# Performance work log

Hardware: AMD Instinct MI355X
Metric: run time of the kernel (lower is better)

## Reference

```python
import jax, jax.numpy as jnp
import numpy as np

EMB = 1024
HEADS = 16
DH = EMB // HEADS


def setup_inputs() -> dict:
    key = jax.random.key(0)
    ks = jax.random.split(key, 9)
    B, S = 4, 2048
    scale = 1.0 / np.sqrt(EMB)
    x = jax.random.normal(ks[0], (B, S, EMB), dtype=jnp.float32)
    Wq = jax.random.normal(ks[1], (EMB, EMB), dtype=jnp.float32) * scale
    Wk = jax.random.normal(ks[2], (EMB, EMB), dtype=jnp.float32) * scale
    Wv = jax.random.normal(ks[3], (EMB, EMB), dtype=jnp.float32) * scale
    Wo = jax.random.normal(ks[4], (EMB, EMB), dtype=jnp.float32) * scale
    bq = jnp.zeros((EMB,), jnp.float32)
    bk = jnp.zeros((EMB,), jnp.float32)
    bv = jnp.zeros((EMB,), jnp.float32)
    bo = jnp.zeros((EMB,), jnp.float32)
    return {"x": x, "Wq": Wq, "bq": bq, "Wk": Wk, "bk": bk,
            "Wv": Wv, "bv": bv, "Wo": Wo, "bo": bo}


def _split_heads(t):
    B, S, _ = t.shape
    return t.reshape(B, S, HEADS, DH).transpose(0, 2, 1, 3)  # [B,H,S,Dh]


def reference(x, Wq, bq, Wk, bk, Wv, bv, Wo, bo):
    q = _split_heads(x @ Wq + bq)
    k = _split_heads(x @ Wk + bk)
    v = _split_heads(x @ Wv + bv)
    # scaled dot-product attention, full [B,H,S,S] score matrix as in source
    logits = jnp.einsum("bhqd,bhkd->bhqk", q, k) / jnp.sqrt(jnp.float32(DH))
    attn = jax.nn.softmax(logits, axis=-1)
    ctx = jnp.einsum("bhqk,bhkd->bhqd", attn, v)
    B, _, S, _ = ctx.shape
    concat = ctx.transpose(0, 2, 1, 3).reshape(B, S, EMB)
    return concat @ Wo + bo
```

## Files before the change

### kernel.cpp

```cpp
#include <hip/hip_runtime.h>
#include <hip/hip_bf16.h>
#include <stdint.h>

typedef __bf16 bf16;
typedef __bf16 bf16x4 __attribute__((ext_vector_type(4)));
typedef __bf16 bf16x8 __attribute__((ext_vector_type(8)));
typedef float f32x4 __attribute__((ext_vector_type(4)));

__device__ __forceinline__ void async_ld16(const void* g, void* l) {
  __builtin_amdgcn_global_load_lds(
      (__attribute__((address_space(1))) void*)(void*)(g),
      (__attribute__((address_space(3))) void*)(l), 16, 0, 0);
}

__device__ __forceinline__ bf16 fast_bf16(float f) {
  uint32_t u = (__float_as_uint(f) + 0x8000u) >> 16;
  union { uint16_t s; bf16 b; } cv;
  cv.s = (uint16_t)u;
  return cv.b;
}

__device__ __forceinline__ uint32_t pack_bf16(float lo, float hi) {
  return __builtin_amdgcn_perm(__float_as_uint(hi) + 0x8000u,
                               __float_as_uint(lo) + 0x8000u, 0x07060302u);
}

__global__ __launch_bounds__(256) void cast_f32_bf16(const float* __restrict__ in,
                                                     bf16* __restrict__ out, int n) {
  int i = (blockIdx.x * 256 + threadIdx.x) * 4;
  if (i < n) {
    float4 f = *(const float4*)(in + i);
    uint2 o;
    o.x = pack_bf16(f.x, f.y);
    o.y = pack_bf16(f.z, f.w);
    *(uint2*)(out + i) = o;
  }
}

__global__ __launch_bounds__(256) void transpose_weights(const float* __restrict__ Wq,
                                                         const float* __restrict__ Wk,
                                                         const float* __restrict__ Wv,
                                                         const float* __restrict__ Wo,
                                                         bf16* __restrict__ Wt,
                                                         bf16* __restrict__ Wot) {
  __shared__ bf16 tile[64][66];
  int z = blockIdx.z;
  const float* src = z == 0 ? Wq : (z == 1 ? Wk : (z == 2 ? Wv : Wo));
  bf16* dst = z == 0 ? Wt : (z == 1 ? Wt + 1048576 : (z == 2 ? Wt + 2097152 : Wot));
  int r0 = blockIdx.x * 64, c0 = blockIdx.y * 64;
  int t = threadIdx.x;
#pragma unroll
  for (int i = 0; i < 16; ++i) {
    int idx = t + i * 256;
    int r = idx >> 6, c = idx & 63;
    tile[r][c] = fast_bf16(src[(size_t)(r0 + r) * 1024 + (c0 + c)]);
  }
  __syncthreads();
#pragma unroll
  for (int i = 0; i < 16; ++i) {
    int idx = t + i * 256;
    int c = idx >> 6, r = idx & 63;
    dst[(size_t)(c0 + c) * 1024 + (r0 + r)] = tile[r][c];
  }
}

__device__ __forceinline__ void gemm128_mainloop(const bf16* __restrict__ A,
                                                 const bf16* __restrict__ Bt, int K,
                                                 int rowBase, int colBase,
                                                 bf16* As, bf16* Bs,
                                                 f32x4 (&acc)[4][4]) {
  int t = threadIdx.x, lane = t & 63, w = t >> 6;
  int wM = w >> 1, wN = w & 1, quad = lane >> 4, l15 = lane & 15;
  int r_off = lane >> 3;
  int c_sw = (((lane & 7) ^ r_off) << 3);
  int sw = l15 & 7;
  for (int k0 = 0; k0 < K; k0 += 64) {
    __syncthreads();
#pragma unroll
    for (int i = 0; i < 4; ++i) {
      int e = i * 2048 + w * 512;
      int row = (e >> 6) + r_off;
      async_ld16(A + (size_t)(rowBase + row) * K + (k0 + c_sw), As + e);
      async_ld16(Bt + (size_t)(colBase + row) * K + (k0 + c_sw), Bs + e);
    }
    __syncthreads();
#pragma unroll
    for (int ks = 0; ks < 2; ++ks) {
      int co = (((ks * 4 + quad) ^ sw) << 3);
      bf16x8 af[4], bfr[4];
#pragma unroll
      for (int mi = 0; mi < 4; ++mi)
        af[mi] = *(const bf16x8*)(As + (wM * 64 + mi * 16 + l15) * 64 + co);
#pragma unroll
      for (int ni = 0; ni < 4; ++ni)
        bfr[ni] = *(const bf16x8*)(Bs + (wN * 64 + ni * 16 + l15) * 64 + co);
#pragma unroll
      for (int mi = 0; mi < 4; ++mi)
#pragma unroll
        for (int ni = 0; ni < 4; ++ni)
          acc[mi][ni] = __builtin_amdgcn_mfma_f32_16x16x32_bf16(af[mi], bfr[ni], acc[mi][ni], 0, 0, 0);
    }
  }
}

__global__ __launch_bounds__(256) void gemm_qkv(const bf16* __restrict__ X,
                                                const bf16* __restrict__ Wt,
                                                const float* __restrict__ bq,
                                                const float* __restrict__ bk,
                                                const float* __restrict__ bv,
                                                bf16* __restrict__ Qo,
                                                bf16* __restrict__ Ko,
                                                bf16* __restrict__ Vto) {
  __shared__ alignas(16) bf16 smem[2 * 128 * 64];
  bf16* As = smem;
  bf16* Bs = smem + 128 * 64;
  f32x4 acc[4][4];
  f32x4 z = {0.f, 0.f, 0.f, 0.f};
#pragma unroll
  for (int mi = 0; mi < 4; ++mi)
#pragma unroll
    for (int ni = 0; ni < 4; ++ni) acc[mi][ni] = z;
  int rowBase = blockIdx.y * 128, colBase = blockIdx.x * 128;
  gemm128_mainloop(X, Wt, 1024, rowBase, colBase, As, Bs, acc);

  int t = threadIdx.x, lane = t & 63, w = t >> 6;
  int wM = w >> 1, wN = w & 1, quad = lane >> 4, l15 = lane & 15;
  int which = colBase >> 10;
  int baseh = (colBase & 1023) >> 6;
  int b = rowBase >> 11, s0 = rowBase & 2047;

  if (which == 2) {
#pragma unroll
    for (int hp = 0; hp < 2; ++hp) {
      __syncthreads();
      if (wN == hp) {
#pragma unroll
        for (int mi = 0; mi < 4; ++mi)
#pragma unroll
          for (int ni = 0; ni < 4; ++ni) {
            int d = ni * 16 + l15;
            float bb = bv[(colBase & 1023) + hp * 64 + d];
            int sl = wM * 64 + mi * 16 + quad * 4;
            uint2 pv;
            pv.x = pack_bf16(acc[mi][ni][0] + bb, acc[mi][ni][1] + bb);
            pv.y = pack_bf16(acc[mi][ni][2] + bb, acc[mi][ni][3] + bb);
            *(uint2*)(smem + d * 136 + sl) = pv;
          }
      }
      __syncthreads();
      int hg = baseh + hp;
#pragma unroll
      for (int it = 0; it < 4; ++it) {
        int idx = t + it * 256;
        int d = idx >> 4, c = idx & 15;
        bf16x8 vv = *(const bf16x8*)(smem + d * 136 + c * 8);
        *(bf16x8*)(Vto + (((size_t)((b << 4) + hg) << 6) + d) * 2048 + s0 + c * 8) = vv;
      }
    }
  } else {
    const float* bias = which == 0 ? bq : bk;
    bf16* dst = which == 0 ? Qo : Ko;
    float scale = which == 0 ? 0.125f * 1.44269504f : 1.0f;
#pragma unroll
    for (int hp = 0; hp < 2; ++hp) {
      __syncthreads();
      if (wN == hp) {
#pragma unroll
        for (int mi = 0; mi < 4; ++mi)
#pragma unroll
          for (int ni = 0; ni < 4; ++ni) {
            int d = ni * 16 + l15;
            float bb = bias[(colBase & 1023) + hp * 64 + d];
            int m = wM * 64 + mi * 16 + quad * 4;
#pragma unroll
            for (int r = 0; r < 4; ++r)
              smem[(m + r) * 72 + d] = fast_bf16((acc[mi][ni][r] + bb) * scale);
          }
      }
      __syncthreads();
      int hg = baseh + hp;
      bf16* gbase = dst + ((((size_t)((b << 4) + hg)) * 2048 + s0) << 6);
#pragma unroll
      for (int it = 0; it < 4; ++it) {
        int idx = t + it * 256;
        int m = idx >> 3, c = idx & 7;
        bf16x8 vv = *(const bf16x8*)(smem + m * 72 + c * 8);
        *(bf16x8*)(gbase + m * 64 + c * 8) = vv;
      }
    }
  }
}

__global__ __launch_bounds__(256) void gemm_out(const bf16* __restrict__ Cb,
                                                const bf16* __restrict__ Wot,
                                                const float* __restrict__ bo,
                                                float* __restrict__ out) {
  __shared__ alignas(16) bf16 As[128 * 64];
  __shared__ alignas(16) bf16 Bs[128 * 64];
  f32x4 acc[4][4];
  f32x4 z = {0.f, 0.f, 0.f, 0.f};
#pragma unroll
  for (int mi = 0; mi < 4; ++mi)
#pragma unroll
    for (int ni = 0; ni < 4; ++ni) acc[mi][ni] = z;
  int rowBase = blockIdx.y * 128, colBase = blockIdx.x * 128;
  gemm128_mainloop(Cb, Wot, 1024, rowBase, colBase, As, Bs, acc);

  int t = threadIdx.x, lane = t & 63, w = t >> 6;
  int wM = w >> 1, wN = w & 1, quad = lane >> 4, l15 = lane & 15;
#pragma unroll
  for (int mi = 0; mi < 4; ++mi)
#pragma unroll
    for (int ni = 0; ni < 4; ++ni) {
      int n = colBase + wN * 64 + ni * 16 + l15;
      float bb = bo[n];
#pragma unroll
      for (int r = 0; r < 4; ++r) {
        int m = rowBase + wM * 64 + mi * 16 + quad * 4 + r;
        out[(size_t)m * 1024 + n] = acc[mi][ni][r] + bb;
      }
    }
}

__global__ __launch_bounds__(256, 2) void attn(const bf16* __restrict__ Q,
                                               const bf16* __restrict__ Kg,
                                               const bf16* __restrict__ Vt,
                                               bf16* __restrict__ ctx) {
  __shared__ alignas(16) bf16 QPs[256 * 64];
  __shared__ alignas(16) bf16 Ks[2][4096];
  __shared__ alignas(16) bf16 Vs[2][4096];

  int t = threadIdx.x, lane = t & 63, w = t >> 6;
  int quad = lane >> 4, l15 = lane & 15;
  int r_off = lane >> 3;
  int c_sw = (((lane & 7) ^ r_off) << 3);
  int sw = l15 & 7;
  int bh = blockIdx.x;
  int q0 = blockIdx.y * 256;
  const bf16* Qp = Q + ((size_t)bh * 2048 + q0) * 64;
  const bf16* Kp = Kg + (size_t)bh * 2048 * 64;
  const bf16* Vp = Vt + (size_t)bh * 64 * 2048;

#pragma unroll
  for (int i = 0; i < 8; ++i) {
    int e = w * 4096 + i * 512;
    int row = (e >> 6) + r_off;
    async_ld16(Qp + (size_t)row * 64 + c_sw, QPs + e);
  }
#pragma unroll
  for (int i = 0; i < 2; ++i) {
    int e = w * 1024 + i * 512;
    int row = (e >> 6) + r_off;
    async_ld16(Kp + (size_t)row * 64 + c_sw, Ks[0] + e);
    async_ld16(Vp + (size_t)row * 2048 + c_sw, Vs[0] + e);
  }
  __syncthreads();

  bf16x8 qf[2][4];
#pragma unroll
  for (int ks = 0; ks < 2; ++ks)
#pragma unroll
    for (int qi = 0; qi < 4; ++qi)
      qf[ks][qi] = *(const bf16x8*)(QPs + (w * 64 + qi * 16 + l15) * 64 + (((ks * 4 + quad) ^ sw) << 3));
  asm volatile("s_waitcnt lgkmcnt(0)" ::: "memory");

  bf16* Ps = QPs + w * 4096;

  bf16 one1 = (bf16)1.0f;
  bf16x8 ones = {one1, one1, one1, one1, one1, one1, one1, one1};

  f32x4 o[4][4];
  f32x4 ol[4];
  f32x4 z = {0.f, 0.f, 0.f, 0.f};
#pragma unroll
  for (int mi = 0; mi < 4; ++mi) {
    ol[mi] = z;
#pragma unroll
    for (int ni = 0; ni < 4; ++ni) o[mi][ni] = z;
  }

  for (int kt = 0; kt < 32; ++kt) {
    int cur = kt & 1;
    if (kt < 31) {
      int kn = (kt + 1) * 64;
#pragma unroll
      for (int i = 0; i < 2; ++i) {
        int e = w * 1024 + i * 512;
        int row = (e >> 6) + r_off;
        async_ld16(Kp + (size_t)(kn + row) * 64 + c_sw, Ks[cur ^ 1] + e);
        async_ld16(Vp + (size_t)row * 2048 + kn + c_sw, Vs[cur ^ 1] + e);
      }
    }
    const bf16* Kc = Ks[cur];
    const bf16* Vc = Vs[cur];

    f32x4 sA[2][4];
#pragma unroll
    for (int ki = 0; ki < 2; ++ki)
#pragma unroll
      for (int qi = 0; qi < 4; ++qi) sA[ki][qi] = z;
#pragma unroll
    for (int ks = 0; ks < 2; ++ks) {
      int co = (((ks * 4 + quad) ^ sw) << 3);
      bf16x8 kf0 = *(const bf16x8*)(Kc + (l15) * 64 + co);
      bf16x8 kf1 = *(const bf16x8*)(Kc + (16 + l15) * 64 + co);
#pragma unroll
      for (int qi = 0; qi < 4; ++qi) {
        sA[0][qi] = __builtin_amdgcn_mfma_f32_16x16x32_bf16(kf0, qf[ks][qi], sA[0][qi], 0, 0, 0);
        sA[1][qi] = __builtin_amdgcn_mfma_f32_16x16x32_bf16(kf1, qf[ks][qi], sA[1][qi], 0, 0, 0);
      }
    }
#pragma unroll
    for (int qi = 0; qi < 4; ++qi)
#pragma unroll
      for (int ki = 0; ki < 2; ++ki) {
        float p0 = __builtin_amdgcn_exp2f(sA[ki][qi][0]);
        float p1 = __builtin_amdgcn_exp2f(sA[ki][qi][1]);
        float p2 = __builtin_amdgcn_exp2f(sA[ki][qi][2]);
        float p3 = __builtin_amdgcn_exp2f(sA[ki][qi][3]);
        uint2 pb;
        pb.x = pack_bf16(p0, p1);
        pb.y = pack_bf16(p2, p3);
        int cs = (ki * 2 + (quad >> 1)) ^ sw;
        *(uint2*)(Ps + (qi * 16 + l15) * 64 + cs * 8 + (quad & 1) * 4) = pb;
      }

    f32x4 sB[2][4];
#pragma unroll
    for (int ki = 0; ki < 2; ++ki)
#pragma unroll
      for (int qi = 0; qi < 4; ++qi) sB[ki][qi] = z;
#pragma unroll
    for (int ks = 0; ks < 2; ++ks) {
      int co = (((ks * 4 + quad) ^ sw) << 3);
      bf16x8 kf2 = *(const bf16x8*)(Kc + (32 + l15) * 64 + co);
      bf16x8 kf3 = *(const bf16x8*)(Kc + (48 + l15) * 64 + co);
#pragma unroll
      for (int qi = 0; qi < 4; ++qi) {
        sB[0][qi] = __builtin_amdgcn_mfma_f32_16x16x32_bf16(kf2, qf[ks][qi], sB[0][qi], 0, 0, 0);
        sB[1][qi] = __builtin_amdgcn_mfma_f32_16x16x32_bf16(kf3, qf[ks][qi], sB[1][qi], 0, 0, 0);
      }
    }

    asm volatile("s_waitcnt lgkmcnt(0)" ::: "memory");

    {
      int co = ((quad ^ sw) << 3);
      bf16x8 pf[4], vf[4];
#pragma unroll
      for (int mi = 0; mi < 4; ++mi)
        pf[mi] = *(const bf16x8*)(Ps + (mi * 16 + l15) * 64 + co);
#pragma unroll
      for (int ni = 0; ni < 4; ++ni)
        vf[ni] = *(const bf16x8*)(Vc + (ni * 16 + l15) * 64 + co);
#pragma unroll
      for (int mi = 0; mi < 4; ++mi) {
#pragma unroll
        for (int ni = 0; ni < 4; ++ni)
          o[mi][ni] = __builtin_amdgcn_mfma_f32_16x16x32_bf16(pf[mi], vf[ni], o[mi][ni], 0, 0, 0);
        ol[mi] = __builtin_amdgcn_mfma_f32_16x16x32_bf16(pf[mi], ones, ol[mi], 0, 0, 0);
      }
    }

#pragma unroll
    for (int qi = 0; qi < 4; ++qi)
#pragma unroll
      for (int ki = 0; ki < 2; ++ki) {
        float p0 = __builtin_amdgcn_exp2f(sB[ki][qi][0]);
        float p1 = __builtin_amdgcn_exp2f(sB[ki][qi][1]);
        float p2 = __builtin_amdgcn_exp2f(sB[ki][qi][2]);
        float p3 = __builtin_amdgcn_exp2f(sB[ki][qi][3]);
        uint2 pb;
        pb.x = pack_bf16(p0, p1);
        pb.y = pack_bf16(p2, p3);
        int cs = (ki * 2 + 4 + (quad >> 1)) ^ sw;
        *(uint2*)(Ps + (qi * 16 + l15) * 64 + cs * 8 + (quad & 1) * 4) = pb;
      }

    asm volatile("s_waitcnt lgkmcnt(0)" ::: "memory");

    {
      int co = (((4 + quad) ^ sw) << 3);
      bf16x8 pf[4], vf[4];
#pragma unroll
      for (int mi = 0; mi < 4; ++mi)
        pf[mi] = *(const bf16x8*)(Ps + (mi * 16 + l15) * 64 + co);
#pragma unroll
      for (int ni = 0; ni < 4; ++ni)
        vf[ni] = *(const bf16x8*)(Vc + (ni * 16 + l15) * 64 + co);
#pragma unroll
      for (int mi = 0; mi < 4; ++mi) {
#pragma unroll
        for (int ni = 0; ni < 4; ++ni)
          o[mi][ni] = __builtin_amdgcn_mfma_f32_16x16x32_bf16(pf[mi], vf[ni], o[mi][ni], 0, 0, 0);
        ol[mi] = __builtin_amdgcn_mfma_f32_16x16x32_bf16(pf[mi], ones, ol[mi], 0, 0, 0);
      }
    }

    __syncthreads();
  }

  int b = bh >> 4, h = bh & 15;
#pragma unroll
  for (int mi = 0; mi < 4; ++mi) {
    float rl[4];
#pragma unroll
    for (int r = 0; r < 4; ++r) rl[r] = 1.0f / ol[mi][r];
#pragma unroll
    for (int ni = 0; ni < 4; ++ni) {
      int col = h * 64 + ni * 16 + l15;
#pragma unroll
      for (int r = 0; r < 4; ++r) {
        int q = q0 + w * 64 + mi * 16 + quad * 4 + r;
        ctx[(size_t)(b * 2048 + q) * 1024 + col] = fast_bf16(o[mi][ni][r] * rl[r]);
      }
    }
  }
}

extern "C" void kernel_launch(void* const* d_in, const int* in_sizes, int n_in,
                              void* d_out, int out_size, void* d_ws, size_t ws_size,
                              hipStream_t stream) {
  const float* x  = (const float*)d_in[0];
  const float* Wq = (const float*)d_in[1];
  const float* bq = (const float*)d_in[2];
  const float* Wk = (const float*)d_in[3];
  const float* bk = (const float*)d_in[4];
  const float* Wv = (const float*)d_in[5];
  const float* bv = (const float*)d_in[6];
  const float* Wo = (const float*)d_in[7];
  const float* bo = (const float*)d_in[8];
  float* out = (float*)d_out;

  char* ws = (char*)d_ws;
  const size_t MB = 1048576;
  bf16* xb  = (bf16*)(ws);
  bf16* Wt  = (bf16*)(ws + 16 * MB);
  bf16* Wot = (bf16*)(ws + 22 * MB);
  bf16* Qb  = (bf16*)(ws + 24 * MB);
  bf16* Kb  = (bf16*)(ws + 40 * MB);
  bf16* Vtb = (bf16*)(ws + 56 * MB);
  bf16* Cx  = (bf16*)(ws + 72 * MB);

  cast_f32_bf16<<<8192, 256, 0, stream>>>(x, xb, 8388608);
  transpose_weights<<<dim3(16, 16, 4), 256, 0, stream>>>(Wq, Wk, Wv, Wo, Wt, Wot);
  gemm_qkv<<<dim3(24, 64, 1), 256, 0, stream>>>(xb, Wt, bq, bk, bv, Qb, Kb, Vtb);
  attn<<<dim3(64, 8, 1), 256, 0, stream>>>(Qb, Kb, Vtb, Cx);
  gemm_out<<<dim3(8, 64, 1), 256, 0, stream>>>(Cx, Wot, bo, out);
}
```

Before: 278.6 us.

## Halve attention query tile, prefetch K/V via registers, raise occupancy with setprio

The attention kernel now processes 128 queries per block instead of 256 (32 rows per wave), doubling the grid and raising the launch-bounds occupancy target from 2 to 4 blocks per CU. The double-buffered async global-to-LDS K/V loads are replaced by a single LDS buffer, with the next tile held in registers and written to LDS between two barriers. s_setprio raises wave priority around MFMA bursts. The aim is more concurrent waves to hide latency, at the cost of halving K/V reuse per block, doubling K/V global traffic, and adding an extra barrier per iteration.

```diff
diff --git a/kernel.cpp b/kernel.cpp
--- a/kernel.cpp
+++ b/kernel.cpp
@@ -222,13 +222,13 @@
     }
 }
 
-__global__ __launch_bounds__(256, 2) void attn(const bf16* __restrict__ Q,
+__global__ __launch_bounds__(256, 4) void attn(const bf16* __restrict__ Q,
                                                const bf16* __restrict__ Kg,
                                                const bf16* __restrict__ Vt,
                                                bf16* __restrict__ ctx) {
-  __shared__ alignas(16) bf16 QPs[256 * 64];
-  __shared__ alignas(16) bf16 Ks[2][4096];
-  __shared__ alignas(16) bf16 Vs[2][4096];
+  __shared__ alignas(16) bf16 QPs[128 * 64];
+  __shared__ alignas(16) bf16 Ks[4096];
+  __shared__ alignas(16) bf16 Vs[4096];
 
   int t = threadIdx.x, lane = t & 63, w = t >> 6;
   int quad = lane >> 4, l15 = lane & 15;
@@ -236,14 +236,14 @@
   int c_sw = (((lane & 7) ^ r_off) << 3);
   int sw = l15 & 7;
   int bh = blockIdx.x;
-  int q0 = blockIdx.y * 256;
+  int q0 = blockIdx.y * 128;
   const bf16* Qp = Q + ((size_t)bh * 2048 + q0) * 64;
   const bf16* Kp = Kg + (size_t)bh * 2048 * 64;
   const bf16* Vp = Vt + (size_t)bh * 64 * 2048;
 
 #pragma unroll
-  for (int i = 0; i < 8; ++i) {
-    int e = w * 4096 + i * 512;
+  for (int i = 0; i < 4; ++i) {
+    int e = w * 2048 + i * 512;
     int row = (e >> 6) + r_off;
     async_ld16(Qp + (size_t)row * 64 + c_sw, QPs + e);
   }
@@ -251,67 +251,67 @@
   for (int i = 0; i < 2; ++i) {
     int e = w * 1024 + i * 512;
     int row = (e >> 6) + r_off;
-    async_ld16(Kp + (size_t)row * 64 + c_sw, Ks[0] + e);
-    async_ld16(Vp + (size_t)row * 2048 + c_sw, Vs[0] + e);
+    async_ld16(Kp + (size_t)row * 64 + c_sw, Ks + e);
+    async_ld16(Vp + (size_t)row * 2048 + c_sw, Vs + e);
   }
   __syncthreads();
 
-  bf16x8 qf[2][4];
+  bf16x8 qf[2][2];
 #pragma unroll
   for (int ks = 0; ks < 2; ++ks)
 #pragma unroll
-    for (int qi = 0; qi < 4; ++qi)
-      qf[ks][qi] = *(const bf16x8*)(QPs + (w * 64 + qi * 16 + l15) * 64 + (((ks * 4 + quad) ^ sw) << 3));
+    for (int qi = 0; qi < 2; ++qi)
+      qf[ks][qi] = *(const bf16x8*)(QPs + (w * 32 + qi * 16 + l15) * 64 + (((ks * 4 + quad) ^ sw) << 3));
   asm volatile("s_waitcnt lgkmcnt(0)" ::: "memory");
 
-  bf16* Ps = QPs + w * 4096;
+  bf16* Ps = QPs + w * 2048;
 
   bf16 one1 = (bf16)1.0f;
   bf16x8 ones = {one1, one1, one1, one1, one1, one1, one1, one1};
 
-  f32x4 o[4][4];
-  f32x4 ol[4];
+  f32x4 o[2][4];
+  f32x4 ol[2];
   f32x4 z = {0.f, 0.f, 0.f, 0.f};
 #pragma unroll
-  for (int mi = 0; mi < 4; ++mi) {
+  for (int mi = 0; mi < 2; ++mi) {
     ol[mi] = z;
 #pragma unroll
     for (int ni = 0; ni < 4; ++ni) o[mi][ni] = z;
   }
 
   for (int kt = 0; kt < 32; ++kt) {
-    int cur = kt & 1;
+    bf16x8 kpre[2], vpre[2];
     if (kt < 31) {
       int kn = (kt + 1) * 64;
 #pragma unroll
       for (int i = 0; i < 2; ++i) {
         int e = w * 1024 + i * 512;
         int row = (e >> 6) + r_off;
-        async_ld16(Kp + (size_t)(kn + row) * 64 + c_sw, Ks[cur ^ 1] + e);
-        async_ld16(Vp + (size_t)row * 2048 + kn + c_sw, Vs[cur ^ 1] + e);
-      }
-    }
-    const bf16* Kc = Ks[cur];
-    const bf16* Vc = Vs[cur];
-
-    f32x4 sA[2][4];
+        kpre[i] = *(const bf16x8*)(Kp + (size_t)(kn + row) * 64 + c_sw);
+        vpre[i] = *(const bf16x8*)(Vp + (size_t)row * 2048 + kn + c_sw);
+      }
+    }
+
+    f32x4 sA[2][2];
 #pragma unroll
     for (int ki = 0; ki < 2; ++ki)
 #pragma unroll
-      for (int qi = 0; qi < 4; ++qi) sA[ki][qi] = z;
+      for (int qi = 0; qi < 2; ++qi) sA[ki][qi] = z;
+    __builtin_amdgcn_s_setprio(1);
 #pragma unroll
     for (int ks = 0; ks < 2; ++ks) {
       int co = (((ks * 4 + quad) ^ sw) << 3);
-      bf16x8 kf0 = *(const bf16x8*)(Kc + (l15) * 64 + co);
-      bf16x8 kf1 = *(const bf16x8*)(Kc + (16 + l15) * 64 + co);
-#pragma unroll
-      for (int qi = 0; qi < 4; ++qi) {
+      bf16x8 kf0 = *(const bf16x8*)(Ks + (l15) * 64 + co);
+      bf16x8 kf1 = *(const bf16x8*)(Ks + (16 + l15) * 64 + co);
+#pragma unroll
+      for (int qi = 0; qi < 2; ++qi) {
         sA[0][qi] = __builtin_amdgcn_mfma_f32_16x16x32_bf16(kf0, qf[ks][qi], sA[0][qi], 0, 0, 0);
         sA[1][qi] = __builtin_amdgcn_mfma_f32_16x16x32_bf16(kf1, qf[ks][qi], sA[1][qi], 0, 0, 0);
       }
     }
-#pragma unroll
-    for (int qi = 0; qi < 4; ++qi)
+    __builtin_amdgcn_s_setprio(0);
+#pragma unroll
+    for (int qi = 0; qi < 2; ++qi)
 #pragma unroll
       for (int ki = 0; ki < 2; ++ki) {
         float p0 = __builtin_amdgcn_exp2f(sA[ki][qi][0]);
@@ -325,45 +325,49 @@
         *(uint2*)(Ps + (qi * 16 + l15) * 64 + cs * 8 + (quad & 1) * 4) = pb;
       }
 
-    f32x4 sB[2][4];
+    f32x4 sB[2][2];
 #pragma unroll
     for (int ki = 0; ki < 2; ++ki)
 #pragma unroll
-      for (int qi = 0; qi < 4; ++qi) sB[ki][qi] = z;
+      for (int qi = 0; qi < 2; ++qi) sB[ki][qi] = z;
+    __builtin_amdgcn_s_setprio(1);
 #pragma unroll
     for (int ks = 0; ks < 2; ++ks) {
       int co = (((ks * 4 + quad) ^ sw) << 3);
-      bf16x8 kf2 = *(const bf16x8*)(Kc + (32 + l15) * 64 + co);
-      bf16x8 kf3 = *(const bf16x8*)(Kc + (48 + l15) * 64 + co);
-#pragma unroll
-      for (int qi = 0; qi < 4; ++qi) {
+      bf16x8 kf2 = *(const bf16x8*)(Ks + (32 + l15) * 64 + co);
+      bf16x8 kf3 = *(const bf16x8*)(Ks + (48 + l15) * 64 + co);
+#pragma unroll
+      for (int qi = 0; qi < 2; ++qi) {
         sB[0][qi] = __builtin_amdgcn_mfma_f32_16x16x32_bf16(kf2, qf[ks][qi], sB[0][qi], 0, 0, 0);
         sB[1][qi] = __builtin_amdgcn_mfma_f32_16x16x32_bf16(kf3, qf[ks][qi], sB[1][qi], 0, 0, 0);
       }
     }
+    __builtin_amdgcn_s_setprio(0);
 
     asm volatile("s_waitcnt lgkmcnt(0)" ::: "memory");
 
     {
       int co = ((quad ^ sw) << 3);
-      bf16x8 pf[4], vf[4];
-#pragma unroll
-      for (int mi = 0; mi < 4; ++mi)
+      bf16x8 pf[2], vf[4];
+#pragma unroll
+      for (int mi = 0; mi < 2; ++mi)
         pf[mi] = *(const bf16x8*)(Ps + (mi * 16 + l15) * 64 + co);
 #pragma unroll
       for (int ni = 0; ni < 4; ++ni)
-        vf[ni] = *(const bf16x8*)(Vc + (ni * 16 + l15) * 64 + co);
-#pragma unroll
-      for (int mi = 0; mi < 4; ++mi) {
+        vf[ni] = *(const bf16x8*)(Vs + (ni * 16 + l15) * 64 + co);
+      __builtin_amdgcn_s_setprio(1);
+#pragma unroll
+      for (int mi = 0; mi < 2; ++mi) {
 #pragma unroll
         for (int ni = 0; ni < 4; ++ni)
           o[mi][ni] = __builtin_amdgcn_mfma_f32_16x16x32_bf16(pf[mi], vf[ni], o[mi][ni], 0, 0, 0);
         ol[mi] = __builtin_amdgcn_mfma_f32_16x16x32_bf16(pf[mi], ones, ol[mi], 0, 0, 0);
       }
-    }
-
-#pragma unroll
-    for (int qi = 0; qi < 4; ++qi)
+      __builtin_amdgcn_s_setprio(0);
+    }
+
+#pragma unroll
+    for (int qi = 0; qi < 2; ++qi)
 #pragma unroll
       for (int ki = 0; ki < 2; ++ki) {
         float p0 = __builtin_amdgcn_exp2f(sB[ki][qi][0]);
@@ -381,28 +385,39 @@
 
     {
       int co = (((4 + quad) ^ sw) << 3);
-      bf16x8 pf[4], vf[4];
-#pragma unroll
-      for (int mi = 0; mi < 4; ++mi)
+      bf16x8 pf[2], vf[4];
+#pragma unroll
+      for (int mi = 0; mi < 2; ++mi)
         pf[mi] = *(const bf16x8*)(Ps + (mi * 16 + l15) * 64 + co);
 #pragma unroll
       for (int ni = 0; ni < 4; ++ni)
-        vf[ni] = *(const bf16x8*)(Vc + (ni * 16 + l15) * 64 + co);
-#pragma unroll
-      for (int mi = 0; mi < 4; ++mi) {
+        vf[ni] = *(const bf16x8*)(Vs + (ni * 16 + l15) * 64 + co);
+      __builtin_amdgcn_s_setprio(1);
+#pragma unroll
+      for (int mi = 0; mi < 2; ++mi) {
 #pragma unroll
         for (int ni = 0; ni < 4; ++ni)
           o[mi][ni] = __builtin_amdgcn_mfma_f32_16x16x32_bf16(pf[mi], vf[ni], o[mi][ni], 0, 0, 0);
         ol[mi] = __builtin_amdgcn_mfma_f32_16x16x32_bf16(pf[mi], ones, ol[mi], 0, 0, 0);
       }
+      __builtin_amdgcn_s_setprio(0);
     }
 
     __syncthreads();
+    if (kt < 31) {
+#pragma unroll
+      for (int i = 0; i < 2; ++i) {
+        int e = w * 1024 + i * 512;
+        *(bf16x8*)(Ks + e + lane * 8) = kpre[i];
+        *(bf16x8*)(Vs + e + lane * 8) = vpre[i];
+      }
+    }
+    __syncthreads();
   }
 
   int b = bh >> 4, h = bh & 15;
 #pragma unroll
-  for (int mi = 0; mi < 4; ++mi) {
+  for (int mi = 0; mi < 2; ++mi) {
     float rl[4];
 #pragma unroll
     for (int r = 0; r < 4; ++r) rl[r] = 1.0f / ol[mi][r];
@@ -411,7 +426,7 @@
       int col = h * 64 + ni * 16 + l15;
 #pragma unroll
       for (int r = 0; r < 4; ++r) {
-        int q = q0 + w * 64 + mi * 16 + quad * 4 + r;
+        int q = q0 + w * 32 + mi * 16 + quad * 4 + r;
         ctx[(size_t)(b * 2048 + q) * 1024 + col] = fast_bf16(o[mi][ni][r] * rl[r]);
       }
     }
@@ -445,6 +460,6 @@
   cast_f32_bf16<<<8192, 256, 0, stream>>>(x, xb, 8388608);
   transpose_weights<<<dim3(16, 16, 4), 256, 0, stream>>>(Wq, Wk, Wv, Wo, Wt, Wot);
   gemm_qkv<<<dim3(24, 64, 1), 256, 0, stream>>>(xb, Wt, bq, bk, bv, Qb, Kb, Vtb);
-  attn<<<dim3(64, 8, 1), 256, 0, stream>>>(Qb, Kb, Vtb, Cx);
+  attn<<<dim3(64, 16, 1), 256, 0, stream>>>(Qb, Kb, Vtb, Cx);
   gemm_out<<<dim3(8, 64, 1), 256, 0, stream>>>(Cx, Wot, bo, out);
 }
```

New measurement: 288.4 us. 1.03x slower.
